# Kernel optimization log

Measured on AMD Instinct MI355X. Metric: run time of the kernel, lower is better.

The kernel has to match this reference:

```python
import jax, jax.numpy as jnp
import numpy as np

D_MODEL = 1024
HIDDEN = 4096
N_EXPERTS = 8
TOP_K = 2


def setup_inputs() -> dict:
    key = jax.random.key(0)
    ks = jax.random.split(key, 7)
    x = jax.random.normal(ks[0], (4, 2048, D_MODEL), dtype=jnp.float32)
    s = 0.02
    Wg = jax.random.normal(ks[1], (D_MODEL, N_EXPERTS), dtype=jnp.float32) * s
    bg = jnp.zeros((N_EXPERTS,), dtype=jnp.float32)
    W1 = jax.random.normal(ks[2], (N_EXPERTS, D_MODEL, HIDDEN), dtype=jnp.float32) * s
    b1 = jnp.zeros((N_EXPERTS, HIDDEN), dtype=jnp.float32)
    W2 = jax.random.normal(ks[3], (N_EXPERTS, HIDDEN, D_MODEL), dtype=jnp.float32) * s
    b2 = jnp.zeros((N_EXPERTS, D_MODEL), dtype=jnp.float32)
    return {"x": x, "Wg": Wg, "bg": bg, "W1": W1, "b1": b1, "W2": W2, "b2": b2}


def reference(x, Wg, bg, W1, b1, W2, b2):
    B, T, D = x.shape
    xf = x.reshape(-1, D)                      # (N, D)
    N = xf.shape[0]

    # --- top-k gate ---
    logits = xf @ Wg + bg                      # (N, E)
    all_probs = jax.nn.softmax(logits, axis=-1)
    topk_logits, topk_idx = jax.lax.top_k(logits, TOP_K)   # (N, k)
    topk_gates = jax.nn.softmax(topk_logits, axis=-1)      # (N, k), sums to 1

    # scatter gates into dense (N, E) masks (matches torch scatter_add_)
    rows = jnp.arange(N)[:, None]
    gate_mask = jnp.zeros((N, N_EXPERTS), dtype=xf.dtype).at[rows, topk_idx].add(topk_gates)
    dispatch_mask = jnp.zeros((N, N_EXPERTS), dtype=xf.dtype).at[rows, topk_idx].add(1.0)

    # --- experts: dense batched form; unselected tokens have gate 0 so math matches ---
    h = jnp.einsum('nd,edh->neh', xf, W1) + b1             # (N, E, H)
    h = jax.nn.relu(h)
    y = jnp.einsum('neh,ehd->ned', h, W2) + b2             # (N, E, D)
    out = jnp.einsum('ned,ne->nd', y, gate_mask)           # weighted combine
    outputs = out.reshape(B, T, D)

    # --- load-balance loss + metadata ---
    tokens_per_expert = (dispatch_mask > 0).sum(axis=0)
    assignment_fraction = gate_mask.sum(axis=0) / N
    expected_prob = all_probs.mean(axis=0)
    load_balance_loss = (expected_prob * assignment_fraction).sum() * N_EXPERTS

    return (outputs, load_balance_loss, tokens_per_expert, expected_prob, assignment_fraction)
```

## Files before the change

kernel.cpp:

```cpp
#include <hip/hip_runtime.h>
#include <stdint.h>

#define D_MODEL 1024
#define HID     4096
#define NE      8
#define NTOK    8192
#define NSLOT   (NTOK*2)
#define TM      128
#define MAX_RB  136
#define MPAD    (MAX_RB*TM)
#define HHALF   2048
#define GATE_BLOCKS 32

typedef unsigned short u16;
typedef __attribute__((ext_vector_type(8))) __bf16 bf16x8;
typedef __attribute__((ext_vector_type(4))) float  f32x4;

__device__ __forceinline__ u16 f2bu(float f){
  uint32_t u = __builtin_bit_cast(uint32_t, f);
  uint32_t r = (u + 0x7FFFu + ((u >> 16) & 1u)) >> 16;
  return (u16)r;
}

__device__ __forceinline__ void gload16(const u16* src, u16* lds){
  __builtin_amdgcn_global_load_lds((const __attribute__((address_space(1))) void*)src,
                                   (__attribute__((address_space(3))) void*)lds, 16, 0, 0);
}

__device__ __forceinline__ int xcd_swz(int w, int nwg){
  int q = nwg >> 3;
  return (w & 7) * q + (w >> 3);
}

#define WAITV(n) do{ asm volatile("s_waitcnt vmcnt(" #n ")" ::: "memory"); \
                     __builtin_amdgcn_sched_barrier(0); }while(0)
#define BARX()   do{ __builtin_amdgcn_sched_barrier(0); \
                     __builtin_amdgcn_s_barrier(); \
                     __builtin_amdgcn_sched_barrier(0); }while(0)

__global__ __launch_bounds__(256) void xcvt_kernel(const float* __restrict__ x, u16* __restrict__ x16){
  size_t i = (size_t)blockIdx.x*256 + threadIdx.x;
  const float4* p = (const float4*)(x + i*8);
  float4 a = p[0], b = p[1];
  u16 o[8] = {f2bu(a.x),f2bu(a.y),f2bu(a.z),f2bu(a.w),f2bu(b.x),f2bu(b.y),f2bu(b.z),f2bu(b.w)};
  *(int4*)(x16 + i*8) = *(int4*)o;
}

__global__ __launch_bounds__(256) void transpose_cvt(const float* __restrict__ in,
                                                     u16* __restrict__ out, int R, int C)
{
  __shared__ float tile[32][33];
  int e = blockIdx.z;
  int r0 = blockIdx.y * 32, c0 = blockIdx.x * 32;
  const float* src = in + (size_t)e * R * C;
  u16* dst = out + (size_t)e * R * C;
  int tx = threadIdx.x, ty = threadIdx.y;
#pragma unroll
  for (int i = 0; i < 4; i++){
    int r = r0 + ty + i*8;
    tile[ty + i*8][tx] = src[(size_t)r * C + c0 + tx];
  }
  __syncthreads();
#pragma unroll
  for (int i = 0; i < 4; i++){
    int c = c0 + ty + i*8;
    dst[(size_t)c * R + r0 + tx] = f2bu(tile[tx][ty + i*8]);
  }
}

__global__ __launch_bounds__(256) void gate_kernel(
    const float* __restrict__ x, const float* __restrict__ Wg, const float* __restrict__ bg,
    int* __restrict__ topk, float* __restrict__ gates,
    float* __restrict__ part_probs, float* __restrict__ part_assign, int* __restrict__ part_cnt)
{
  __shared__ float sp[256][8];
  __shared__ float sa[256][8];
  __shared__ int   sc[256][8];
  int t = threadIdx.x;
  int n = blockIdx.x * 256 + t;
  float lg[8];
#pragma unroll
  for (int e = 0; e < 8; e++) lg[e] = bg[e];
  const float4* xr = (const float4*)(x + (size_t)n * D_MODEL);
  for (int j = 0; j < D_MODEL/4; j++){
    float4 v = xr[j];
    const float* wr = Wg + (size_t)j * 32;
#pragma unroll
    for (int e = 0; e < 8; e++)
      lg[e] += v.x*wr[e] + v.y*wr[8+e] + v.z*wr[16+e] + v.w*wr[24+e];
  }
  float m = lg[0];
#pragma unroll
  for (int e = 1; e < 8; e++) m = fmaxf(m, lg[e]);
  float p[8]; float s = 0.f;
#pragma unroll
  for (int e = 0; e < 8; e++){ p[e] = expf(lg[e]-m); s += p[e]; }
  float inv = 1.f / s;
  int bi = 0; float best = lg[0];
#pragma unroll
  for (int e = 1; e < 8; e++) if (lg[e] > best){ best = lg[e]; bi = e; }
  int bi2 = 0; float best2 = -3.0e38f;
#pragma unroll
  for (int e = 0; e < 8; e++) if (e != bi && lg[e] > best2){ best2 = lg[e]; bi2 = e; }
  float t1 = expf(best2 - best);
  float g0 = 1.f / (1.f + t1);
  float g1 = t1 / (1.f + t1);
  topk[2*n] = bi;  topk[2*n+1] = bi2;
  gates[2*n] = g0; gates[2*n+1] = g1;
#pragma unroll
  for (int e = 0; e < 8; e++){
    sp[t][e] = p[e] * inv;
    sa[t][e] = (e == bi) ? g0 : ((e == bi2) ? g1 : 0.f);
    sc[t][e] = (e == bi || e == bi2) ? 1 : 0;
  }
  __syncthreads();
  if (t < 8){
    float s2 = 0.f; for (int i = 0; i < 256; i++) s2 += sp[i][t];
    part_probs[blockIdx.x*8 + t] = s2;
  } else if (t < 16){
    int e = t - 8; float s2 = 0.f; for (int i = 0; i < 256; i++) s2 += sa[i][e];
    part_assign[blockIdx.x*8 + e] = s2;
  } else if (t < 24){
    int e = t - 16; int c = 0; for (int i = 0; i < 256; i++) c += sc[i][e];
    part_cnt[blockIdx.x*8 + e] = c;
  }
}

__global__ __launch_bounds__(256) void scan_kernel(const int* __restrict__ part_cnt,
                                                   int* __restrict__ counts,
                                                   int* __restrict__ padded_off,
                                                   int* __restrict__ cursor,
                                                   int* __restrict__ block_expert,
                                                   int* __restrict__ routed)
{
  __shared__ int off[NE+1];
  int t = threadIdx.x;
  if (t == 0){
    int o = 0; off[0] = 0;
    for (int e = 0; e < NE; e++){
      int c = 0;
      for (int b = 0; b < GATE_BLOCKS; b++) c += part_cnt[b*8 + e];
      counts[e] = c;
      o += ((c + TM - 1) / TM) * TM;
      off[e+1] = o;
    }
    for (int e = 0; e <= NE; e++) padded_off[e] = off[e];
  }
  __syncthreads();
  if (t < NE) cursor[t] = 0;
  for (int rb = t; rb < MAX_RB; rb += 256){
    int e = -1;
    int r = rb * TM;
    for (int j = 0; j < NE; j++)
      if (r >= off[j] && r < off[j+1]) e = j;
    block_expert[rb] = e;
  }
  for (int i = t; i < MPAD; i += 256) routed[i] = -1;
}

__global__ __launch_bounds__(256) void place_kernel(const int* __restrict__ topk,
                                                    const int* __restrict__ padded_off,
                                                    int* __restrict__ cursor,
                                                    int* __restrict__ routed)
{
  int s = blockIdx.x * 256 + threadIdx.x;
  int e = topk[s];
  int pos = padded_off[e] + atomicAdd(&cursor[e], 1);
  routed[pos] = s;
}

__global__ __launch_bounds__(256, 3) void gemm1_kernel(
    const u16* __restrict__ x16, const u16* __restrict__ w1t, const float* __restrict__ b1,
    const int* __restrict__ routed, const int* __restrict__ block_expert,
    u16* __restrict__ h, int half)
{
  int l = xcd_swz(blockIdx.x, gridDim.x);
  int rb = l >> 4, cb = l & 15;
  int e = block_expert[rb];
  if (e < 0) return;
  __shared__ __align__(16) u16 Al[3][128][32];
  __shared__ __align__(16) u16 Bl[3][128][32];
  u16* AF = &Al[0][0][0];
  u16* BF = &Bl[0][0][0];
  int t = threadIdx.x;
  int lane = t & 63, wid = t >> 6;

  int srow0 = wid*32 + (lane >> 2);
  int sch = ((lane & 3) ^ ((lane >> 3) & 3)) * 8;

  int slot0 = routed[rb*TM + srow0];
  int slot1 = routed[rb*TM + srow0 + 16];
  int tok0 = slot0 >= 0 ? (slot0 >> 1) : 0;
  int tok1 = slot1 >= 0 ? (slot1 >> 1) : 0;
  const u16* srcA0 = x16 + (size_t)tok0 * D_MODEL + sch;
  const u16* srcA1 = x16 + (size_t)tok1 * D_MODEL + sch;
  const u16* wb = w1t + ((size_t)e*HID + (size_t)half*HHALF + (size_t)cb*128) * D_MODEL + sch;
  const u16* srcB0 = wb + (size_t)srow0 * D_MODEL;
  const u16* srcB1 = wb + (size_t)(srow0 + 16) * D_MODEL;

  int wr = wid >> 1, wc = wid & 1;
  int fr = lane & 15, fk = lane >> 4;
  int fkx8 = (fk ^ ((fr >> 1) & 3)) * 8;
  f32x4 acc[4][4];
#pragma unroll
  for (int i = 0; i < 4; i++)
#pragma unroll
    for (int j = 0; j < 4; j++) acc[i][j] = (f32x4){0.f,0.f,0.f,0.f};

#define STG1(bo, kk) do{ \
    gload16(srcA0 + (kk), AF + (bo) + wid*1024); \
    gload16(srcA1 + (kk), AF + (bo) + wid*1024 + 512); \
    gload16(srcB0 + (kk), BF + (bo) + wid*1024); \
    gload16(srcB1 + (kk), BF + (bo) + wid*1024 + 512); } while(0)

#define CMP1(bo) do{ \
    bf16x8 af[4], bf[4]; \
    _Pragma("unroll") \
    for (int mm = 0; mm < 4; mm++) af[mm] = *(const bf16x8*)(AF + (bo) + (wr*64 + mm*16 + fr)*32 + fkx8); \
    _Pragma("unroll") \
    for (int nn = 0; nn < 4; nn++) bf[nn] = *(const bf16x8*)(BF + (bo) + (wc*64 + nn*16 + fr)*32 + fkx8); \
    _Pragma("unroll") \
    for (int mm = 0; mm < 4; mm++) \
      _Pragma("unroll") \
      for (int nn = 0; nn < 4; nn++) \
        acc[mm][nn] = __builtin_amdgcn_mfma_f32_16x16x32_bf16(af[mm], bf[nn], acc[mm][nn], 0, 0, 0); } while(0)

  const int nk = D_MODEL/32;
  STG1(0, 0); STG1(4096, 32); STG1(8192, 64);
  int bo = 0;
  for (int i = 0; i < nk - 2; i++){
    WAITV(8);
    BARX();
    CMP1(bo);
    BARX();
    if (i < nk - 3) STG1(bo, (i+3)*32);
    bo = (bo == 8192) ? 0 : bo + 4096;
  }
  WAITV(4); BARX(); CMP1(bo); BARX();
  bo = (bo == 8192) ? 0 : bo + 4096;
  WAITV(0); BARX(); CMP1(bo);

  int r4 = fk * 4;
#pragma unroll
  for (int nn = 0; nn < 4; nn++){
    int ct = wc*64 + nn*16 + fr;
    float bias = b1[(size_t)e*HID + (size_t)half*HHALF + cb*128 + ct];
#pragma unroll
    for (int mm = 0; mm < 4; mm++){
#pragma unroll
      for (int r = 0; r < 4; r++){
        int rt = wr*64 + mm*16 + r4 + r;
        float v = acc[mm][nn][r] + bias;
        v = v > 0.f ? v : 0.f;
        h[(size_t)(rb*TM + rt) * HHALF + cb*128 + ct] = f2bu(v);
      }
    }
  }
#undef STG1
#undef CMP1
}

__global__ __launch_bounds__(256, 3) void gemm2_kernel(
    const u16* __restrict__ h, const u16* __restrict__ w2t,
    const int* __restrict__ routed, const int* __restrict__ block_expert,
    const float* __restrict__ gates, float* __restrict__ y, int half)
{
  int l = xcd_swz(blockIdx.x, gridDim.x);
  int rb = l >> 3, cb = l & 7;
  int e = block_expert[rb];
  if (e < 0) return;
  __shared__ __align__(16) u16 Al[3][128][32];
  __shared__ __align__(16) u16 Bl[3][128][32];
  __shared__ int   rslot[128];
  __shared__ float rgate[128];
  u16* AF = &Al[0][0][0];
  u16* BF = &Bl[0][0][0];
  int t = threadIdx.x;
  int lane = t & 63, wid = t >> 6;
  if (t < 128){
    int s = routed[rb*TM + t];
    rslot[t] = s;
    rgate[t] = (s >= 0) ? gates[s] : 0.f;
  }

  int srow0 = wid*32 + (lane >> 2);
  int sch = ((lane & 3) ^ ((lane >> 3) & 3)) * 8;
  const u16* srcA0 = h + (size_t)(rb*TM + srow0) * HHALF + sch;
  const u16* srcA1 = h + (size_t)(rb*TM + srow0 + 16) * HHALF + sch;
  const u16* wb = w2t + ((size_t)e*D_MODEL + (size_t)cb*128) * HID + (size_t)half*HHALF + sch;
  const u16* srcB0 = wb + (size_t)srow0 * HID;
  const u16* srcB1 = wb + (size_t)(srow0 + 16) * HID;

  int wr = wid >> 1, wc = wid & 1;
  int fr = lane & 15, fk = lane >> 4;
  int fkx8 = (fk ^ ((fr >> 1) & 3)) * 8;
  f32x4 acc[4][4];
#pragma unroll
  for (int i = 0; i < 4; i++)
#pragma unroll
    for (int j = 0; j < 4; j++) acc[i][j] = (f32x4){0.f,0.f,0.f,0.f};

#define STG2(bo, kk) do{ \
    gload16(srcA0 + (kk), AF + (bo) + wid*1024); \
    gload16(srcA1 + (kk), AF + (bo) + wid*1024 + 512); \
    gload16(srcB0 + (kk), BF + (bo) + wid*1024); \
    gload16(srcB1 + (kk), BF + (bo) + wid*1024 + 512); } while(0)

#define CMP2(bo) do{ \
    bf16x8 af[4], bf[4]; \
    _Pragma("unroll") \
    for (int mm = 0; mm < 4; mm++) af[mm] = *(const bf16x8*)(AF + (bo) + (wr*64 + mm*16 + fr)*32 + fkx8); \
    _Pragma("unroll") \
    for (int nn = 0; nn < 4; nn++) bf[nn] = *(const bf16x8*)(BF + (bo) + (wc*64 + nn*16 + fr)*32 + fkx8); \
    _Pragma("unroll") \
    for (int mm = 0; mm < 4; mm++) \
      _Pragma("unroll") \
      for (int nn = 0; nn < 4; nn++) \
        acc[mm][nn] = __builtin_amdgcn_mfma_f32_16x16x32_bf16(af[mm], bf[nn], acc[mm][nn], 0, 0, 0); } while(0)

  const int nk = HHALF/32;
  STG2(0, 0); STG2(4096, 32); STG2(8192, 64);
  int bo = 0;
  for (int i = 0; i < nk - 2; i++){
    WAITV(8);
    BARX();
    CMP2(bo);
    BARX();
    if (i < nk - 3) STG2(bo, (i+3)*32);
    bo = (bo == 8192) ? 0 : bo + 4096;
  }
  WAITV(4); BARX(); CMP2(bo); BARX();
  bo = (bo == 8192) ? 0 : bo + 4096;
  WAITV(0); BARX(); CMP2(bo);

  int r4 = fk * 4;
#pragma unroll
  for (int mm = 0; mm < 4; mm++){
#pragma unroll
    for (int r = 0; r < 4; r++){
      int rt = wr*64 + mm*16 + r4 + r;
      int slot = rslot[rt];
      if (slot < 0) continue;
      float g = rgate[rt];
#pragma unroll
      for (int nn = 0; nn < 4; nn++){
        int ct = wc*64 + nn*16 + fr;
        size_t idx = (size_t)slot * D_MODEL + cb*128 + ct;
        float val = g * acc[mm][nn][r];
        if (half == 0) y[idx] = val;
        else           y[idx] += val;
      }
    }
  }
#undef STG2
#undef CMP2
}

__global__ __launch_bounds__(256) void combine_kernel(
    const float* __restrict__ y, const int* __restrict__ topk, const float* __restrict__ gates,
    const float* __restrict__ b2, float* __restrict__ out)
{
  int i = blockIdx.x * 256 + threadIdx.x;
  int n = i >> 8;
  int d = (i & 255) * 4;
  float4 a  = *(const float4*)(y + (size_t)(2*n)   * D_MODEL + d);
  float4 b  = *(const float4*)(y + (size_t)(2*n+1) * D_MODEL + d);
  int e0 = topk[2*n], e1 = topk[2*n+1];
  float g0 = gates[2*n], g1 = gates[2*n+1];
  float4 c0 = *(const float4*)(b2 + (size_t)e0 * D_MODEL + d);
  float4 c1 = *(const float4*)(b2 + (size_t)e1 * D_MODEL + d);
  float4 o;
  o.x = a.x + b.x + g0*c0.x + g1*c1.x;
  o.y = a.y + b.y + g0*c0.y + g1*c1.y;
  o.z = a.z + b.z + g0*c0.z + g1*c1.z;
  o.w = a.w + b.w + g0*c0.w + g1*c1.w;
  *(float4*)(out + (size_t)n * D_MODEL + d) = o;
}

__global__ void finalize_kernel(const float* __restrict__ part_probs,
                                const float* __restrict__ part_assign,
                                const int* __restrict__ counts,
                                float* __restrict__ out_tail)
{
  __shared__ float ep[8], af[8];
  int t = threadIdx.x;
  if (t < 8){
    float s = 0.f;
    for (int b = 0; b < GATE_BLOCKS; b++) s += part_probs[b*8 + t];
    ep[t] = s / (float)NTOK;
  } else if (t < 16){
    int e = t - 8; float s = 0.f;
    for (int b = 0; b < GATE_BLOCKS; b++) s += part_assign[b*8 + e];
    af[e] = s / (float)NTOK;
  }
  __syncthreads();
  if (t == 0){
    float loss = 0.f;
    for (int e = 0; e < 8; e++) loss += ep[e] * af[e];
    out_tail[0] = loss * (float)NE;
  }
  if (t < 8){
    out_tail[1 + t]  = (float)counts[t];
    out_tail[9 + t]  = ep[t];
    out_tail[17 + t] = af[t];
  }
}

extern "C" void kernel_launch(void* const* d_in, const int* in_sizes, int n_in,
                              void* d_out, int out_size, void* d_ws, size_t ws_size,
                              hipStream_t stream)
{
  const float* x  = (const float*)d_in[0];
  const float* Wg = (const float*)d_in[1];
  const float* bg = (const float*)d_in[2];
  const float* W1 = (const float*)d_in[3];
  const float* b1 = (const float*)d_in[4];
  const float* W2 = (const float*)d_in[5];
  const float* b2 = (const float*)d_in[6];
  float* out = (float*)d_out;

  char* ws = (char*)d_ws;
  size_t o = 0;
  auto alloc = [&](size_t bytes) -> char* {
    char* p = ws + o; o = (o + bytes + 255) & ~(size_t)255; return p;
  };
  int*   topk        = (int*)   alloc((size_t)NSLOT*4);
  float* gates       = (float*) alloc((size_t)NSLOT*4);
  int*   counts      = (int*)   alloc(NE*4);
  int*   padded_off  = (int*)   alloc((NE+1)*4);
  int*   cursor      = (int*)   alloc(NE*4);
  int*   block_exp   = (int*)   alloc(MAX_RB*4);
  int*   routed      = (int*)   alloc((size_t)MPAD*4);
  float* part_probs  = (float*) alloc(GATE_BLOCKS*8*4);
  float* part_assign = (float*) alloc(GATE_BLOCKS*8*4);
  int*   part_cnt    = (int*)   alloc(GATE_BLOCKS*8*4);
  u16*   x16         = (u16*)   alloc((size_t)NTOK*D_MODEL*2);
  u16*   w1t         = (u16*)   alloc((size_t)NE*HID*D_MODEL*2);
  u16*   w2t         = (u16*)   alloc((size_t)NE*HID*D_MODEL*2);
  u16*   hbuf        = (u16*)   alloc((size_t)MPAD*HHALF*2);
  float* ybuf        = (float*) alloc((size_t)NSLOT*D_MODEL*4);
  (void)ws_size; (void)in_sizes; (void)n_in; (void)out_size;

  transpose_cvt<<<dim3(HID/32, D_MODEL/32, NE), dim3(32,8), 0, stream>>>(W1, w1t, D_MODEL, HID);
  transpose_cvt<<<dim3(D_MODEL/32, HID/32, NE), dim3(32,8), 0, stream>>>(W2, w2t, HID, D_MODEL);
  xcvt_kernel<<<(NTOK*D_MODEL)/(256*8), 256, 0, stream>>>(x, x16);
  gate_kernel<<<GATE_BLOCKS, 256, 0, stream>>>(x, Wg, bg, topk, gates, part_probs, part_assign, part_cnt);
  scan_kernel<<<1, 256, 0, stream>>>(part_cnt, counts, padded_off, cursor, block_exp, routed);
  place_kernel<<<NSLOT/256, 256, 0, stream>>>(topk, padded_off, cursor, routed);
  for (int half = 0; half < 2; half++){
    gemm1_kernel<<<16*MAX_RB, 256, 0, stream>>>(x16, w1t, b1, routed, block_exp, hbuf, half);
    gemm2_kernel<<<8*MAX_RB, 256, 0, stream>>>(hbuf, w2t, routed, block_exp, gates, ybuf, half);
  }
  combine_kernel<<<NTOK, 256, 0, stream>>>(ybuf, topk, gates, b2, out);
  finalize_kernel<<<1, 64, 0, stream>>>(part_probs, part_assign, counts, out + (size_t)NTOK*D_MODEL);
}
```

Baseline: 677.9 us.

## Vectorize weight transpose, fuse x conversion into gate, store partial outputs in bf16

The weight transpose-convert kernel now uses 64x32 tiles, float4 loads and 16-byte packed bf16 stores instead of scalar accesses. The separate x-to-bf16 conversion kernel is removed and the conversion is done inside the gate kernel while it already streams x. The per-slot expert output buffer changes from fp32 to bf16, halving its write/read traffic in gemm2 and combine. The cost is an extra bf16 rounding of the partial sums across the two hidden halves, and a gate kernel with only 32 blocks now also carries the x16 writes.

```diff
diff --git a/kernel.cpp b/kernel.cpp
--- a/kernel.cpp
+++ b/kernel.cpp
@@ -21,6 +21,10 @@
   uint32_t r = (u + 0x7FFFu + ((u >> 16) & 1u)) >> 16;
   return (u16)r;
 }
+__device__ __forceinline__ float b2f(u16 v){
+  uint32_t u = ((uint32_t)v) << 16;
+  return __builtin_bit_cast(float, u);
+}
 
 __device__ __forceinline__ void gload16(const u16* src, u16* lds){
   __builtin_amdgcn_global_load_lds((const __attribute__((address_space(1))) void*)src,
@@ -38,39 +42,36 @@
                      __builtin_amdgcn_s_barrier(); \
                      __builtin_amdgcn_sched_barrier(0); }while(0)
 
-__global__ __launch_bounds__(256) void xcvt_kernel(const float* __restrict__ x, u16* __restrict__ x16){
-  size_t i = (size_t)blockIdx.x*256 + threadIdx.x;
-  const float4* p = (const float4*)(x + i*8);
-  float4 a = p[0], b = p[1];
-  u16 o[8] = {f2bu(a.x),f2bu(a.y),f2bu(a.z),f2bu(a.w),f2bu(b.x),f2bu(b.y),f2bu(b.z),f2bu(b.w)};
-  *(int4*)(x16 + i*8) = *(int4*)o;
-}
-
 __global__ __launch_bounds__(256) void transpose_cvt(const float* __restrict__ in,
                                                      u16* __restrict__ out, int R, int C)
 {
-  __shared__ float tile[32][33];
+  __shared__ float tile[64][33];
   int e = blockIdx.z;
-  int r0 = blockIdx.y * 32, c0 = blockIdx.x * 32;
+  int r0 = blockIdx.y * 64, c0 = blockIdx.x * 32;
   const float* src = in + (size_t)e * R * C;
   u16* dst = out + (size_t)e * R * C;
-  int tx = threadIdx.x, ty = threadIdx.y;
-#pragma unroll
-  for (int i = 0; i < 4; i++){
-    int r = r0 + ty + i*8;
-    tile[ty + i*8][tx] = src[(size_t)r * C + c0 + tx];
+  int t = threadIdx.x;
+  int rr = t >> 3;
+  int tc4 = (t & 7) * 4;
+#pragma unroll
+  for (int p = 0; p < 2; p++){
+    int r = rr + p*32;
+    float4 v = *(const float4*)(src + (size_t)(r0 + r) * C + c0 + tc4);
+    tile[r][tc4+0] = v.x; tile[r][tc4+1] = v.y;
+    tile[r][tc4+2] = v.z; tile[r][tc4+3] = v.w;
   }
   __syncthreads();
-#pragma unroll
-  for (int i = 0; i < 4; i++){
-    int c = c0 + ty + i*8;
-    dst[(size_t)c * R + r0 + tx] = f2bu(tile[tx][ty + i*8]);
-  }
+  int c = t >> 3;
+  int seg = (t & 7) * 8;
+  u16 o[8];
+#pragma unroll
+  for (int j = 0; j < 8; j++) o[j] = f2bu(tile[seg + j][c]);
+  *(int4*)(dst + (size_t)(c0 + c) * R + r0 + seg) = *(int4*)o;
 }
 
 __global__ __launch_bounds__(256) void gate_kernel(
     const float* __restrict__ x, const float* __restrict__ Wg, const float* __restrict__ bg,
-    int* __restrict__ topk, float* __restrict__ gates,
+    int* __restrict__ topk, float* __restrict__ gates, u16* __restrict__ x16,
     float* __restrict__ part_probs, float* __restrict__ part_assign, int* __restrict__ part_cnt)
 {
   __shared__ float sp[256][8];
@@ -82,12 +83,17 @@
 #pragma unroll
   for (int e = 0; e < 8; e++) lg[e] = bg[e];
   const float4* xr = (const float4*)(x + (size_t)n * D_MODEL);
+  u16* xo = x16 + (size_t)n * D_MODEL;
+  u16 tmp[8];
   for (int j = 0; j < D_MODEL/4; j++){
     float4 v = xr[j];
     const float* wr = Wg + (size_t)j * 32;
 #pragma unroll
     for (int e = 0; e < 8; e++)
       lg[e] += v.x*wr[e] + v.y*wr[8+e] + v.z*wr[16+e] + v.w*wr[24+e];
+    int o4 = (j & 1) * 4;
+    tmp[o4+0] = f2bu(v.x); tmp[o4+1] = f2bu(v.y); tmp[o4+2] = f2bu(v.z); tmp[o4+3] = f2bu(v.w);
+    if (j & 1) *(int4*)(xo + (j-1)*4) = *(int4*)tmp;
   }
   float m = lg[0];
 #pragma unroll
@@ -169,6 +175,7 @@
   routed[pos] = s;
 }
 
+
 __global__ __launch_bounds__(256, 3) void gemm1_kernel(
     const u16* __restrict__ x16, const u16* __restrict__ w1t, const float* __restrict__ b1,
     const int* __restrict__ routed, const int* __restrict__ block_expert,
@@ -263,7 +270,7 @@
 __global__ __launch_bounds__(256, 3) void gemm2_kernel(
     const u16* __restrict__ h, const u16* __restrict__ w2t,
     const int* __restrict__ routed, const int* __restrict__ block_expert,
-    const float* __restrict__ gates, float* __restrict__ y, int half)
+    const float* __restrict__ gates, u16* __restrict__ y, int half)
 {
   int l = xcd_swz(blockIdx.x, gridDim.x);
   int rb = l >> 3, cb = l & 7;
@@ -347,8 +354,8 @@
         int ct = wc*64 + nn*16 + fr;
         size_t idx = (size_t)slot * D_MODEL + cb*128 + ct;
         float val = g * acc[mm][nn][r];
-        if (half == 0) y[idx] = val;
-        else           y[idx] += val;
+        if (half == 0) y[idx] = f2bu(val);
+        else           y[idx] = f2bu(b2f(y[idx]) + val);
       }
     }
   }
@@ -357,23 +364,23 @@
 }
 
 __global__ __launch_bounds__(256) void combine_kernel(
-    const float* __restrict__ y, const int* __restrict__ topk, const float* __restrict__ gates,
+    const u16* __restrict__ y, const int* __restrict__ topk, const float* __restrict__ gates,
     const float* __restrict__ b2, float* __restrict__ out)
 {
   int i = blockIdx.x * 256 + threadIdx.x;
   int n = i >> 8;
   int d = (i & 255) * 4;
-  float4 a  = *(const float4*)(y + (size_t)(2*n)   * D_MODEL + d);
-  float4 b  = *(const float4*)(y + (size_t)(2*n+1) * D_MODEL + d);
+  ushort4 a4 = *(const ushort4*)(y + (size_t)(2*n)   * D_MODEL + d);
+  ushort4 b4 = *(const ushort4*)(y + (size_t)(2*n+1) * D_MODEL + d);
   int e0 = topk[2*n], e1 = topk[2*n+1];
   float g0 = gates[2*n], g1 = gates[2*n+1];
   float4 c0 = *(const float4*)(b2 + (size_t)e0 * D_MODEL + d);
   float4 c1 = *(const float4*)(b2 + (size_t)e1 * D_MODEL + d);
   float4 o;
-  o.x = a.x + b.x + g0*c0.x + g1*c1.x;
-  o.y = a.y + b.y + g0*c0.y + g1*c1.y;
-  o.z = a.z + b.z + g0*c0.z + g1*c1.z;
-  o.w = a.w + b.w + g0*c0.w + g1*c1.w;
+  o.x = b2f(a4.x) + b2f(b4.x) + g0*c0.x + g1*c1.x;
+  o.y = b2f(a4.y) + b2f(b4.y) + g0*c0.y + g1*c1.y;
+  o.z = b2f(a4.z) + b2f(b4.z) + g0*c0.z + g1*c1.z;
+  o.w = b2f(a4.w) + b2f(b4.w) + g0*c0.w + g1*c1.w;
   *(float4*)(out + (size_t)n * D_MODEL + d) = o;
 }
 
@@ -438,13 +445,12 @@
   u16*   w1t         = (u16*)   alloc((size_t)NE*HID*D_MODEL*2);
   u16*   w2t         = (u16*)   alloc((size_t)NE*HID*D_MODEL*2);
   u16*   hbuf        = (u16*)   alloc((size_t)MPAD*HHALF*2);
-  float* ybuf        = (float*) alloc((size_t)NSLOT*D_MODEL*4);
+  u16*   ybuf        = (u16*)   alloc((size_t)NSLOT*D_MODEL*2);
   (void)ws_size; (void)in_sizes; (void)n_in; (void)out_size;
 
-  transpose_cvt<<<dim3(HID/32, D_MODEL/32, NE), dim3(32,8), 0, stream>>>(W1, w1t, D_MODEL, HID);
-  transpose_cvt<<<dim3(D_MODEL/32, HID/32, NE), dim3(32,8), 0, stream>>>(W2, w2t, HID, D_MODEL);
-  xcvt_kernel<<<(NTOK*D_MODEL)/(256*8), 256, 0, stream>>>(x, x16);
-  gate_kernel<<<GATE_BLOCKS, 256, 0, stream>>>(x, Wg, bg, topk, gates, part_probs, part_assign, part_cnt);
+  transpose_cvt<<<dim3(HID/32, D_MODEL/64, NE), 256, 0, stream>>>(W1, w1t, D_MODEL, HID);
+  transpose_cvt<<<dim3(D_MODEL/32, HID/64, NE), 256, 0, stream>>>(W2, w2t, HID, D_MODEL);
+  gate_kernel<<<GATE_BLOCKS, 256, 0, stream>>>(x, Wg, bg, topk, gates, x16, part_probs, part_assign, part_cnt);
   scan_kernel<<<1, 256, 0, stream>>>(part_cnt, counts, padded_off, cursor, block_exp, routed);
   place_kernel<<<NSLOT/256, 256, 0, stream>>>(topk, padded_off, cursor, routed);
   for (int half = 0; half < 2; half++){
```

Measured after the change: 701.6 us. 3.5% more time.
